# Kernel optimization log

Hardware: AMD Instinct MI355X
Metric: run time of the kernel (lower is better)

The kernel has to match this reference:

```python
import jax, jax.numpy as jnp
import numpy as np

B, S, H, D = 256, 512, 512, 1  # batch, seq_len, rnn_hid_size (== S*D), input_dim


def lstm_cell(x, h, c, Wih, Whh, bih, bhh):
    # torch.nn.LSTMCell: gates ordered i, f, g, o
    g = x @ Wih.T + bih + h @ Whh.T + bhh  # [B, 4H]
    i, f, gg, o = jnp.split(g, 4, axis=-1)
    i = jax.nn.sigmoid(i)
    f = jax.nn.sigmoid(f)
    gg = jnp.tanh(gg)
    o = jax.nn.sigmoid(o)
    c_new = f * c + i * gg
    h_new = o * jnp.tanh(c_new)
    return h_new, c_new


def setup_inputs() -> dict:
    key = jax.random.key(0)
    ks = jax.random.split(key, 14)
    sc = 1.0 / np.sqrt(H)  # torch LSTMCell/Linear default uniform bound
    u = lambda k, shape: jax.random.uniform(k, shape, jnp.float32, -sc, sc)
    values = jax.random.normal(ks[0], (B, S), jnp.float32)
    masks = jax.random.randint(ks[1], (B, S), 0, 2).astype(jnp.float32)
    return {
        "values": values,
        "masks": masks,
        "Wih_f": u(ks[2], (4 * H, D)), "Whh_f": u(ks[3], (4 * H, H)),
        "bih_f": u(ks[4], (4 * H,)), "bhh_f": u(ks[5], (4 * H,)),
        "Wih_b": u(ks[6], (4 * H, D)), "Whh_b": u(ks[7], (4 * H, H)),
        "bih_b": u(ks[8], (4 * H,)), "bhh_b": u(ks[9], (4 * H,)),
        "W_imp": u(ks[10], (D, H)), "b_imp": u(ks[11], (D,)),
    }


def reference(values, masks, Wih_f, Whh_f, bih_f, bhh_f,
              Wih_b, Whh_b, bih_b, bhh_b, W_imp, b_imp):
    x_f = values[:, :, None]  # [B, S, 1]
    m_f = masks[:, :, None]
    # flip over axis 2 (size 1) is a no-op, matching the original exactly
    x_b = jnp.flip(x_f, axis=2)
    m_b = jnp.flip(m_f, axis=2)

    start_f = jnp.full((B, D), 128.0, jnp.float32)
    start_b = jnp.full((B, D), -128.0, jnp.float32)
    z = jnp.zeros((B, H), jnp.float32)
    h_f, c_f = lstm_cell(start_f, z, z, Wih_f, Whh_f, bih_f, bhh_f)
    h_b, c_b = lstm_cell(start_b, z, z, Wih_b, Whh_b, bih_b, bhh_b)

    xs = (jnp.swapaxes(x_f, 0, 1), jnp.swapaxes(m_f, 0, 1),
          jnp.swapaxes(x_b, 0, 1), jnp.swapaxes(m_b, 0, 1))  # [S, B, 1] each

    def step(carry, inp):
        hf, cf, hb, cb = carry
        xf, mf, xb, mb = inp
        imp_f = hf @ W_imp.T + b_imp
        imp_b = hb @ W_imp.T + b_imp
        cc_f = (1.0 - mf) * xf + mf * imp_f
        cc_b = (1.0 - mb) * xb + mb * imp_b
        hf, cf = lstm_cell(cc_f, hf, cf, Wih_f, Whh_f, bih_f, bhh_f)
        hb, cb = lstm_cell(cc_b, hb, cb, Wih_b, Whh_b, bih_b, bhh_b)
        return (hf, cf, hb, cb), None

    (h_f, c_f, h_b, c_b), _ = jax.lax.scan(step, (h_f, c_f, h_b, c_b), xs)
    h = h_f + h_b  # [B, H]
    imputations = h.reshape(B, S, D)  # requires H == S * D
    out = imputations * (1.0 - m_f) + x_f * m_f
    return h, out
```

## Files before the change

### kernel.cpp

```cpp
#include <hip/hip_runtime.h>
#include <stdint.h>

#define B_ 256
#define S_ 512
#define H_ 512

typedef __attribute__((ext_vector_type(4))) float f32x4;
typedef __attribute__((ext_vector_type(4))) int   i32x4;
typedef __attribute__((ext_vector_type(8))) short s16x8;

__device__ __forceinline__ short f2bf(float f) {
    union { float f; uint32_t u; } c; c.f = f;
    uint32_t u = c.u;
    u += 0x7fffu + ((u >> 16) & 1u);
    return (short)(u >> 16);
}
__device__ __forceinline__ float sig_(float x)  { return 1.0f / (1.0f + __expf(-x)); }
__device__ __forceinline__ float tanh_(float x) { return 1.0f - 2.0f / (1.0f + __expf(2.0f * x)); }

__device__ __forceinline__ void load_a16(const void* p, i32x4* a) {
    asm volatile(
        "global_load_dwordx4 %0, %16, off sc0 sc1\n\t"
        "global_load_dwordx4 %1, %16, off offset:64 sc0 sc1\n\t"
        "global_load_dwordx4 %2, %16, off offset:128 sc0 sc1\n\t"
        "global_load_dwordx4 %3, %16, off offset:192 sc0 sc1\n\t"
        "global_load_dwordx4 %4, %16, off offset:256 sc0 sc1\n\t"
        "global_load_dwordx4 %5, %16, off offset:320 sc0 sc1\n\t"
        "global_load_dwordx4 %6, %16, off offset:384 sc0 sc1\n\t"
        "global_load_dwordx4 %7, %16, off offset:448 sc0 sc1\n\t"
        "global_load_dwordx4 %8, %16, off offset:512 sc0 sc1\n\t"
        "global_load_dwordx4 %9, %16, off offset:576 sc0 sc1\n\t"
        "global_load_dwordx4 %10, %16, off offset:640 sc0 sc1\n\t"
        "global_load_dwordx4 %11, %16, off offset:704 sc0 sc1\n\t"
        "global_load_dwordx4 %12, %16, off offset:768 sc0 sc1\n\t"
        "global_load_dwordx4 %13, %16, off offset:832 sc0 sc1\n\t"
        "global_load_dwordx4 %14, %16, off offset:896 sc0 sc1\n\t"
        "global_load_dwordx4 %15, %16, off offset:960 sc0 sc1\n\t"
        "s_waitcnt vmcnt(0)"
        : "=v"(a[0]), "=v"(a[1]), "=v"(a[2]), "=v"(a[3]),
          "=v"(a[4]), "=v"(a[5]), "=v"(a[6]), "=v"(a[7]),
          "=v"(a[8]), "=v"(a[9]), "=v"(a[10]), "=v"(a[11]),
          "=v"(a[12]), "=v"(a[13]), "=v"(a[14]), "=v"(a[15])
        : "v"(p)
        : "memory");
}

__device__ __forceinline__ void store_h4(void* p, int h0, int h1, int h2, int h3) {
    asm volatile(
        "global_store_short %4, %0, off sc0 sc1\n\t"
        "global_store_short %4, %1, off offset:1024 sc0 sc1\n\t"
        "global_store_short %4, %2, off offset:2048 sc0 sc1\n\t"
        "global_store_short %4, %3, off offset:3072 sc0 sc1"
        :: "v"(h0), "v"(h1), "v"(h2), "v"(h3), "v"(p)
        : "memory");
}

__global__ void __launch_bounds__(256, 1)
lstm_kernel(const float* __restrict__ values, const float* __restrict__ masks,
            const float* __restrict__ Wih_f, const float* __restrict__ Whh_f,
            const float* __restrict__ bih_f, const float* __restrict__ bhh_f,
            const float* __restrict__ Wih_b, const float* __restrict__ Whh_b,
            const float* __restrict__ bih_b, const float* __restrict__ bhh_b,
            const float* __restrict__ W_imp, const float* __restrict__ b_imp,
            unsigned int* ctrs, short* h_buf, float* hfin)
{
    __shared__ short imp_lds[16 * 64 * 8];
    __shared__ float cc_lds[32];

    const int tid  = threadIdx.x;
    const int lane = tid & 63;
    const int wave = tid >> 6;
    const int mw = wave >> 1;
    const int nw = wave & 1;

    const int bid = blockIdx.x;
    const int xg  = bid & 7;
    const int s_  = bid >> 3;
    const int d   = s_ & 1;
    const int w   = s_ >> 1;
    const int cluster = xg * 2 + d;

    const float* Whh = d ? Whh_b : Whh_f;
    const float* Wih = d ? Wih_b : Wih_f;
    const float* bih = d ? bih_b : bih_f;
    const float* bhh = d ? bhh_b : bhh_f;

    const int col16 = lane & 15;
    const int koff4 = lane >> 4;
    const int jcol  = w * 32 + nw * 16 + col16;

    for (int c = tid; c < 1024; c += 256) {
        int ccol = c & 15, ckoff = (c >> 4) & 3, ckb = c >> 6;
        int k0 = ckb * 32 + ckoff * 8;
        short* dst = &imp_lds[c * 8];
        if (ccol == 0) {
            #pragma unroll
            for (int j = 0; j < 8; ++j) dst[j] = f2bf(W_imp[k0 + j]);
        } else {
            #pragma unroll
            for (int j = 0; j < 8; ++j) dst[j] = 0;
        }
    }

    s16x8 bfr[4][16];
    {
        const float* base = Whh + (size_t)jcol * 512 + koff4 * 8;
        #pragma unroll
        for (int g = 0; g < 4; ++g) {
            const float* src = base + (size_t)g * 512 * 512;
            #pragma unroll
            for (int kb = 0; kb < 16; ++kb) {
                f32x4 v0 = *(const f32x4*)(src + kb * 32);
                f32x4 v1 = *(const f32x4*)(src + kb * 32 + 4);
                s16x8 b;
                b[0] = f2bf(v0[0]); b[1] = f2bf(v0[1]); b[2] = f2bf(v0[2]); b[3] = f2bf(v0[3]);
                b[4] = f2bf(v1[0]); b[5] = f2bf(v1[1]); b[6] = f2bf(v1[2]); b[7] = f2bf(v1[3]);
                bfr[g][kb] = b;
            }
        }
    }

    float bias[4], wih[4];
    #pragma unroll
    for (int g = 0; g < 4; ++g) {
        int gc = g * 512 + jcol;
        bias[g] = bih[gc] + bhh[gc];
        wih[g]  = Wih[gc];
    }
    const float bimp  = b_imp[0];
    const float start = d ? -128.0f : 128.0f;

    unsigned int* ctr = ctrs + cluster * 64;

    const int arow   = xg * 32 + mw * 16 + col16;
    const int rowbase = xg * 32 + mw * 16 + koff4 * 4;
    const int imp_off = (koff4 * 16 + col16) * 8;

    float c_reg[4];
    {
        float pre[4];
        #pragma unroll
        for (int g = 0; g < 4; ++g) pre[g] = start * wih[g] + bias[g];
        float i0 = sig_(pre[0]), g0 = tanh_(pre[2]), o0 = sig_(pre[3]);
        float c0 = i0 * g0;
        float h0 = o0 * tanh_(c0);
        #pragma unroll
        for (int r = 0; r < 4; ++r) c_reg[r] = c0;
        int hb16 = (int)(unsigned short)(unsigned)f2bf(h0);
        short* dst = h_buf + d * (B_ * H_) + (size_t)rowbase * H_ + jcol;
        store_h4(dst, hb16, hb16, hb16, hb16);
    }
    asm volatile("s_waitcnt vmcnt(0)" ::: "memory");
    __syncthreads();
    if (tid == 0) {
        __hip_atomic_fetch_add(ctr, 1u, __ATOMIC_RELAXED, __HIP_MEMORY_SCOPE_AGENT);
        while (__hip_atomic_load(ctr, __ATOMIC_RELAXED, __HIP_MEMORY_SCOPE_AGENT) < 16u)
            __builtin_amdgcn_s_sleep(1);
    }
    __syncthreads();

    for (int t = 0; t < S_; ++t) {
        const int p = t & 1;
        const short* hb_r = h_buf + p       * (2 * B_ * H_) + d * (B_ * H_);
        short*       hb_w = h_buf + (p ^ 1) * (2 * B_ * H_) + d * (B_ * H_);

        float xv[4], mv[4];
        if (nw == 0 && col16 == 0) {
            #pragma unroll
            for (int r = 0; r < 4; ++r) {
                int rabs = rowbase + r;
                xv[r] = values[rabs * S_ + t];
                mv[r] = masks[rabs * S_ + t];
            }
        }

        i32x4 a_regs[16];
        load_a16(hb_r + (size_t)arow * H_ + koff4 * 8, a_regs);

        f32x4 acc0 = {0,0,0,0}, acc1 = {0,0,0,0}, acc2 = {0,0,0,0}, acc3 = {0,0,0,0};
        f32x4 acc4 = {0,0,0,0};
        #pragma unroll
        for (int kb = 0; kb < 16; ++kb) {
            s16x8 a = __builtin_bit_cast(s16x8, a_regs[kb]);
            acc0 = __builtin_amdgcn_mfma_f32_16x16x32_bf16(a, bfr[0][kb], acc0, 0, 0, 0);
            acc1 = __builtin_amdgcn_mfma_f32_16x16x32_bf16(a, bfr[1][kb], acc1, 0, 0, 0);
            acc2 = __builtin_amdgcn_mfma_f32_16x16x32_bf16(a, bfr[2][kb], acc2, 0, 0, 0);
            acc3 = __builtin_amdgcn_mfma_f32_16x16x32_bf16(a, bfr[3][kb], acc3, 0, 0, 0);
            if (nw == 0) {
                s16x8 b4 = *(const s16x8*)&imp_lds[kb * 512 + imp_off];
                acc4 = __builtin_amdgcn_mfma_f32_16x16x32_bf16(a, b4, acc4, 0, 0, 0);
            }
        }

        if (nw == 0 && col16 == 0) {
            #pragma unroll
            for (int r = 0; r < 4; ++r) {
                float imp = acc4[r] + bimp;
                cc_lds[mw * 16 + koff4 * 4 + r] = (1.0f - mv[r]) * xv[r] + mv[r] * imp;
            }
        }
        __syncthreads();

        int hbits[4];
        #pragma unroll
        for (int r = 0; r < 4; ++r) {
            float cc = cc_lds[mw * 16 + koff4 * 4 + r];
            float pi = acc0[r] + cc * wih[0] + bias[0];
            float pf = acc1[r] + cc * wih[1] + bias[1];
            float pg = acc2[r] + cc * wih[2] + bias[2];
            float po = acc3[r] + cc * wih[3] + bias[3];
            float iv = sig_(pi), fv = sig_(pf), gv = tanh_(pg), ov = sig_(po);
            c_reg[r] = fv * c_reg[r] + iv * gv;
            float hn = ov * tanh_(c_reg[r]);
            hbits[r] = (int)(unsigned short)(unsigned)f2bf(hn);
            if (t == S_ - 1) hfin[d * (B_ * H_) + (rowbase + r) * H_ + jcol] = hn;
        }
        store_h4(hb_w + (size_t)rowbase * H_ + jcol, hbits[0], hbits[1], hbits[2], hbits[3]);

        asm volatile("s_waitcnt vmcnt(0)" ::: "memory");
        __syncthreads();
        if (tid == 0) {
            __hip_atomic_fetch_add(ctr, 1u, __ATOMIC_RELAXED, __HIP_MEMORY_SCOPE_AGENT);
            unsigned int tgt = 16u * (unsigned)(t + 2);
            while (__hip_atomic_load(ctr, __ATOMIC_RELAXED, __HIP_MEMORY_SCOPE_AGENT) < tgt)
                __builtin_amdgcn_s_sleep(1);
        }
        __syncthreads();
    }
}

__global__ void __launch_bounds__(256)
epilogue_kernel(const float* __restrict__ values, const float* __restrict__ masks,
                const float* __restrict__ hfin, float* __restrict__ out)
{
    int i = blockIdx.x * 256 + threadIdx.x;
    float h = hfin[i] + hfin[B_ * H_ + i];
    out[i] = h;
    float xv = values[i], mv = masks[i];
    out[B_ * H_ + i] = h * (1.0f - mv) + xv * mv;
}

extern "C" void kernel_launch(void* const* d_in, const int* in_sizes, int n_in,
                              void* d_out, int out_size, void* d_ws, size_t ws_size,
                              hipStream_t stream) {
    const float* values = (const float*)d_in[0];
    const float* masks  = (const float*)d_in[1];
    const float* Wih_f  = (const float*)d_in[2];
    const float* Whh_f  = (const float*)d_in[3];
    const float* bih_f  = (const float*)d_in[4];
    const float* bhh_f  = (const float*)d_in[5];
    const float* Wih_b  = (const float*)d_in[6];
    const float* Whh_b  = (const float*)d_in[7];
    const float* bih_b  = (const float*)d_in[8];
    const float* bhh_b  = (const float*)d_in[9];
    const float* W_imp  = (const float*)d_in[10];
    const float* b_imp  = (const float*)d_in[11];

    unsigned int* ctrs = (unsigned int*)d_ws;
    short* h_buf = (short*)((char*)d_ws + 8192);
    float* hfin  = (float*)((char*)d_ws + 8192 + 2 * 2 * B_ * H_ * sizeof(short));

    hipMemsetAsync(d_ws, 0, 8192, stream);

    void* args[] = {
        (void*)&values, (void*)&masks,
        (void*)&Wih_f, (void*)&Whh_f, (void*)&bih_f, (void*)&bhh_f,
        (void*)&Wih_b, (void*)&Whh_b, (void*)&bih_b, (void*)&bhh_b,
        (void*)&W_imp, (void*)&b_imp,
        (void*)&ctrs, (void*)&h_buf, (void*)&hfin
    };
    hipError_t err = hipLaunchCooperativeKernel((const void*)lstm_kernel,
                                                dim3(256), dim3(256), args, 0, stream);
    if (err != hipSuccess) {
        lstm_kernel<<<dim3(256), dim3(256), 0, stream>>>(
            values, masks, Wih_f, Whh_f, bih_f, bhh_f,
            Wih_b, Whh_b, bih_b, bhh_b, W_imp, b_imp, ctrs, h_buf, hfin);
    }

    epilogue_kernel<<<dim3((B_ * H_) / 256), dim3(256), 0, stream>>>(
        values, masks, hfin, (float*)d_out);
}
```

Before: 2.817 ms.

## Replace atomic counter barrier with per-block flags and pipeline hidden-state loads

Swaps the per-cluster atomic counter barrier for per-block step flags. Each wave polls its 16 peers' flags directly, so the extra __syncthreads and single-thread spin are gone. The 16 hidden-state loads are split into four waitcnt stages interleaved with the MFMAs, and values/masks are pre-packed as bf16 into LDS so they are no longer loaded from global memory every step. The risks are lost precision on x*(1-m) and m from the bf16 packing, and weaker memory ordering since the flag stores are plain stores rather than atomics.

```diff
diff --git a/kernel.cpp b/kernel.cpp
--- a/kernel.cpp
+++ b/kernel.cpp
@@ -4,6 +4,8 @@
 #define B_ 256
 #define S_ 512
 #define H_ 512
+
+#define LDS_BYTES 82176
 
 typedef __attribute__((ext_vector_type(4))) float f32x4;
 typedef __attribute__((ext_vector_type(4))) int   i32x4;
@@ -15,10 +17,12 @@
     u += 0x7fffu + ((u >> 16) & 1u);
     return (short)(u >> 16);
 }
+__device__ __forceinline__ float bflo(uint32_t u) { return __builtin_bit_cast(float, u << 16); }
+__device__ __forceinline__ float bfhi(uint32_t u) { return __builtin_bit_cast(float, u & 0xffff0000u); }
 __device__ __forceinline__ float sig_(float x)  { return 1.0f / (1.0f + __expf(-x)); }
 __device__ __forceinline__ float tanh_(float x) { return 1.0f - 2.0f / (1.0f + __expf(2.0f * x)); }
 
-__device__ __forceinline__ void load_a16(const void* p, i32x4* a) {
+__device__ __forceinline__ void load_a16_issue(const void* p, i32x4* a) {
     asm volatile(
         "global_load_dwordx4 %0, %16, off sc0 sc1\n\t"
         "global_load_dwordx4 %1, %16, off offset:64 sc0 sc1\n\t"
@@ -35,8 +39,7 @@
         "global_load_dwordx4 %12, %16, off offset:768 sc0 sc1\n\t"
         "global_load_dwordx4 %13, %16, off offset:832 sc0 sc1\n\t"
         "global_load_dwordx4 %14, %16, off offset:896 sc0 sc1\n\t"
-        "global_load_dwordx4 %15, %16, off offset:960 sc0 sc1\n\t"
-        "s_waitcnt vmcnt(0)"
+        "global_load_dwordx4 %15, %16, off offset:960 sc0 sc1"
         : "=v"(a[0]), "=v"(a[1]), "=v"(a[2]), "=v"(a[3]),
           "=v"(a[4]), "=v"(a[5]), "=v"(a[6]), "=v"(a[7]),
           "=v"(a[8]), "=v"(a[9]), "=v"(a[10]), "=v"(a[11]),
@@ -44,6 +47,8 @@
         : "v"(p)
         : "memory");
 }
+#define AWAIT(imm, x0, x1, x2, x3) \
+    asm volatile("s_waitcnt vmcnt(" #imm ")" : "+v"(x0), "+v"(x1), "+v"(x2), "+v"(x3) :: "memory")
 
 __device__ __forceinline__ void store_h4(void* p, int h0, int h1, int h2, int h3) {
     asm volatile(
@@ -64,8 +69,12 @@
             const float* __restrict__ W_imp, const float* __restrict__ b_imp,
             unsigned int* ctrs, short* h_buf, float* hfin)
 {
-    __shared__ short imp_lds[16 * 64 * 8];
-    __shared__ float cc_lds[32];
+    extern __shared__ char smem_raw[];
+    short*    imp_lds = (short*)smem_raw;
+    uint32_t* xm_lds  = (uint32_t*)(smem_raw + 16384);
+    float*    cc_lds  = (float*)(smem_raw + 81920);
+
+    uint32_t* flags = (uint32_t*)ctrs + 64;
 
     const int tid  = threadIdx.x;
     const int lane = tid & 63;
@@ -101,6 +110,13 @@
             for (int j = 0; j < 8; ++j) dst[j] = 0;
         }
     }
+    for (int i = tid; i < 32 * 512; i += 256) {
+        int r = i >> 9, s = i & 511;
+        float x = values[(xg * 32 + r) * S_ + s];
+        float m = masks[(xg * 32 + r) * S_ + s];
+        float a = x * (1.0f - m);
+        xm_lds[i] = (uint32_t)(uint16_t)f2bf(a) | ((uint32_t)(uint16_t)f2bf(m) << 16);
+    }
 
     s16x8 bfr[4][16];
     {
@@ -130,11 +146,13 @@
     const float bimp  = b_imp[0];
     const float start = d ? -128.0f : 128.0f;
 
-    unsigned int* ctr = ctrs + cluster * 64;
-
-    const int arow   = xg * 32 + mw * 16 + col16;
-    const int rowbase = xg * 32 + mw * 16 + koff4 * 4;
+    const int arow    = xg * 32 + mw * 16 + col16;
+    const int rowloc  = mw * 16 + koff4 * 4;
+    const int rowbase = xg * 32 + rowloc;
     const int imp_off = (koff4 * 16 + col16) * 8;
+
+    uint32_t* myflag = flags + cluster * 16 + w;
+    const uint32_t* pollp = flags + cluster * 16 + col16;
 
     float c_reg[4];
     {
@@ -152,35 +170,32 @@
     }
     asm volatile("s_waitcnt vmcnt(0)" ::: "memory");
     __syncthreads();
-    if (tid == 0) {
-        __hip_atomic_fetch_add(ctr, 1u, __ATOMIC_RELAXED, __HIP_MEMORY_SCOPE_AGENT);
-        while (__hip_atomic_load(ctr, __ATOMIC_RELAXED, __HIP_MEMORY_SCOPE_AGENT) < 16u)
-            __builtin_amdgcn_s_sleep(1);
-    }
-    __syncthreads();
+    if (tid == 0)
+        asm volatile("global_store_dword %0, %1, off sc0 sc1" :: "v"(myflag), "v"(1u) : "memory");
 
     for (int t = 0; t < S_; ++t) {
         const int p = t & 1;
         const short* hb_r = h_buf + p       * (2 * B_ * H_) + d * (B_ * H_);
         short*       hb_w = h_buf + (p ^ 1) * (2 * B_ * H_) + d * (B_ * H_);
 
-        float xv[4], mv[4];
-        if (nw == 0 && col16 == 0) {
-            #pragma unroll
-            for (int r = 0; r < 4; ++r) {
-                int rabs = rowbase + r;
-                xv[r] = values[rabs * S_ + t];
-                mv[r] = masks[rabs * S_ + t];
+        {
+            const uint32_t tgt = (uint32_t)(t + 1);
+            for (;;) {
+                uint32_t f;
+                asm volatile("global_load_dword %0, %1, off sc0 sc1\n\ts_waitcnt vmcnt(0)"
+                             : "=v"(f) : "v"(pollp) : "memory");
+                if (__ballot(f >= tgt || col16 == w) == ~0ull) break;
             }
         }
 
         i32x4 a_regs[16];
-        load_a16(hb_r + (size_t)arow * H_ + koff4 * 8, a_regs);
+        load_a16_issue(hb_r + (size_t)arow * H_ + koff4 * 8, a_regs);
 
         f32x4 acc0 = {0,0,0,0}, acc1 = {0,0,0,0}, acc2 = {0,0,0,0}, acc3 = {0,0,0,0};
         f32x4 acc4 = {0,0,0,0};
-        #pragma unroll
-        for (int kb = 0; kb < 16; ++kb) {
+        AWAIT(12, a_regs[0], a_regs[1], a_regs[2], a_regs[3]);
+        #pragma unroll
+        for (int kb = 0; kb < 4; ++kb) {
             s16x8 a = __builtin_bit_cast(s16x8, a_regs[kb]);
             acc0 = __builtin_amdgcn_mfma_f32_16x16x32_bf16(a, bfr[0][kb], acc0, 0, 0, 0);
             acc1 = __builtin_amdgcn_mfma_f32_16x16x32_bf16(a, bfr[1][kb], acc1, 0, 0, 0);
@@ -191,12 +206,51 @@
                 acc4 = __builtin_amdgcn_mfma_f32_16x16x32_bf16(a, b4, acc4, 0, 0, 0);
             }
         }
+        AWAIT(8, a_regs[4], a_regs[5], a_regs[6], a_regs[7]);
+        #pragma unroll
+        for (int kb = 4; kb < 8; ++kb) {
+            s16x8 a = __builtin_bit_cast(s16x8, a_regs[kb]);
+            acc0 = __builtin_amdgcn_mfma_f32_16x16x32_bf16(a, bfr[0][kb], acc0, 0, 0, 0);
+            acc1 = __builtin_amdgcn_mfma_f32_16x16x32_bf16(a, bfr[1][kb], acc1, 0, 0, 0);
+            acc2 = __builtin_amdgcn_mfma_f32_16x16x32_bf16(a, bfr[2][kb], acc2, 0, 0, 0);
+            acc3 = __builtin_amdgcn_mfma_f32_16x16x32_bf16(a, bfr[3][kb], acc3, 0, 0, 0);
+            if (nw == 0) {
+                s16x8 b4 = *(const s16x8*)&imp_lds[kb * 512 + imp_off];
+                acc4 = __builtin_amdgcn_mfma_f32_16x16x32_bf16(a, b4, acc4, 0, 0, 0);
+            }
+        }
+        AWAIT(4, a_regs[8], a_regs[9], a_regs[10], a_regs[11]);
+        #pragma unroll
+        for (int kb = 8; kb < 12; ++kb) {
+            s16x8 a = __builtin_bit_cast(s16x8, a_regs[kb]);
+            acc0 = __builtin_amdgcn_mfma_f32_16x16x32_bf16(a, bfr[0][kb], acc0, 0, 0, 0);
+            acc1 = __builtin_amdgcn_mfma_f32_16x16x32_bf16(a, bfr[1][kb], acc1, 0, 0, 0);
+            acc2 = __builtin_amdgcn_mfma_f32_16x16x32_bf16(a, bfr[2][kb], acc2, 0, 0, 0);
+            acc3 = __builtin_amdgcn_mfma_f32_16x16x32_bf16(a, bfr[3][kb], acc3, 0, 0, 0);
+            if (nw == 0) {
+                s16x8 b4 = *(const s16x8*)&imp_lds[kb * 512 + imp_off];
+                acc4 = __builtin_amdgcn_mfma_f32_16x16x32_bf16(a, b4, acc4, 0, 0, 0);
+            }
+        }
+        AWAIT(0, a_regs[12], a_regs[13], a_regs[14], a_regs[15]);
+        #pragma unroll
+        for (int kb = 12; kb < 16; ++kb) {
+            s16x8 a = __builtin_bit_cast(s16x8, a_regs[kb]);
+            acc0 = __builtin_amdgcn_mfma_f32_16x16x32_bf16(a, bfr[0][kb], acc0, 0, 0, 0);
+            acc1 = __builtin_amdgcn_mfma_f32_16x16x32_bf16(a, bfr[1][kb], acc1, 0, 0, 0);
+            acc2 = __builtin_amdgcn_mfma_f32_16x16x32_bf16(a, bfr[2][kb], acc2, 0, 0, 0);
+            acc3 = __builtin_amdgcn_mfma_f32_16x16x32_bf16(a, bfr[3][kb], acc3, 0, 0, 0);
+            if (nw == 0) {
+                s16x8 b4 = *(const s16x8*)&imp_lds[kb * 512 + imp_off];
+                acc4 = __builtin_amdgcn_mfma_f32_16x16x32_bf16(a, b4, acc4, 0, 0, 0);
+            }
+        }
 
         if (nw == 0 && col16 == 0) {
             #pragma unroll
             for (int r = 0; r < 4; ++r) {
-                float imp = acc4[r] + bimp;
-                cc_lds[mw * 16 + koff4 * 4 + r] = (1.0f - mv[r]) * xv[r] + mv[r] * imp;
+                uint32_t pk = xm_lds[(rowloc + r) * 512 + t];
+                cc_lds[rowloc + r] = bflo(pk) + bfhi(pk) * (acc4[r] + bimp);
             }
         }
         __syncthreads();
@@ -204,7 +258,7 @@
         int hbits[4];
         #pragma unroll
         for (int r = 0; r < 4; ++r) {
-            float cc = cc_lds[mw * 16 + koff4 * 4 + r];
+            float cc = cc_lds[rowloc + r];
             float pi = acc0[r] + cc * wih[0] + bias[0];
             float pf = acc1[r] + cc * wih[1] + bias[1];
             float pg = acc2[r] + cc * wih[2] + bias[2];
@@ -219,13 +273,9 @@
 
         asm volatile("s_waitcnt vmcnt(0)" ::: "memory");
         __syncthreads();
-        if (tid == 0) {
-            __hip_atomic_fetch_add(ctr, 1u, __ATOMIC_RELAXED, __HIP_MEMORY_SCOPE_AGENT);
-            unsigned int tgt = 16u * (unsigned)(t + 2);
-            while (__hip_atomic_load(ctr, __ATOMIC_RELAXED, __HIP_MEMORY_SCOPE_AGENT) < tgt)
-                __builtin_amdgcn_s_sleep(1);
-        }
-        __syncthreads();
+        if (tid == 0)
+            asm volatile("global_store_dword %0, %1, off sc0 sc1"
+                         :: "v"(myflag), "v"((uint32_t)(t + 2)) : "memory");
     }
 }
 
@@ -262,6 +312,9 @@
 
     hipMemsetAsync(d_ws, 0, 8192, stream);
 
+    hipFuncSetAttribute((const void*)lstm_kernel,
+                        hipFuncAttributeMaxDynamicSharedMemorySize, LDS_BYTES);
+
     void* args[] = {
         (void*)&values, (void*)&masks,
         (void*)&Wih_f, (void*)&Whh_f, (void*)&bih_f, (void*)&bhh_f,
@@ -270,9 +323,10 @@
         (void*)&ctrs, (void*)&h_buf, (void*)&hfin
     };
     hipError_t err = hipLaunchCooperativeKernel((const void*)lstm_kernel,
-                                                dim3(256), dim3(256), args, 0, stream);
+                                                dim3(256), dim3(256), args,
+                                                (unsigned int)LDS_BYTES, stream);
     if (err != hipSuccess) {
-        lstm_kernel<<<dim3(256), dim3(256), 0, stream>>>(
+        lstm_kernel<<<dim3(256), dim3(256), LDS_BYTES, stream>>>(
             values, masks, Wih_f, Whh_f, bih_f, bhh_f,
             Wih_b, Whh_b, bih_b, bhh_b, W_imp, b_imp, ctrs, h_buf, hfin);
     }
```

Result: slower. 3.789 ms (+34.5%).
